# Optimization experiments

Measured on AMD Instinct MI355X. Metric: run time of the kernel, lower is better.

The kernel has to match this reference:

```python
import jax, jax.numpy as jnp
import numpy as np

PATCH_LEN = 16


def _forward(x, W_proj, b_proj, W_router, b_router, W_experts, b_experts, W_head, b_head):
    # x: (B, L, C); Model drops first 2 channels
    seq_len = x.shape[1]
    xs = x[:, :, 2:]                                   # (B, L, N)
    B, L, N = xs.shape
    # CI=True: 'b l n -> (b n) l 1' (track as (BN, L) since trailing dim is 1)
    ci = jnp.transpose(xs, (0, 2, 1)).reshape(B * N, L)
    # RevIN-style instance norm (means detached in torch)
    means = jax.lax.stop_gradient(jnp.mean(ci, axis=1, keepdims=True))
    xc = ci - means
    stdev = jnp.sqrt(jnp.var(xc, axis=1, keepdims=True) + 1e-5)  # unbiased=False
    xc = xc / stdev
    # non-overlapping patching: unfold(1, pl, pl)
    p = L // PATCH_LEN
    patches = xc[:, : p * PATCH_LEN].reshape(B * N, p, PATCH_LEN)
    xp = patches @ W_proj.T + b_proj                   # (BN, p, d)
    gates = jax.nn.softmax(xp @ W_router.T + b_router, axis=-1)  # (BN, p, E)
    # soft-routed mixture of linear experts: sum_e gate_e * (xp @ W_e^T + b_e)
    eo = jnp.einsum('tpd,ehd->tpeh', xp, W_experts) + b_experts  # (BN, p, E, d)
    combined = jnp.einsum('tpeh,tpe->tph', eo, gates)            # (BN, p, d)
    d = combined.shape[-1]
    flat = combined.reshape(B * N, p * d)              # '(b n) p d -> b (p d) n', n=1
    if p * d < seq_len:
        flat = jnp.pad(flat, ((0, 0), (0, seq_len - p * d)))
    else:
        flat = flat[:, :seq_len]
    flat = flat * stdev + means                        # de-normalize (BN, L)
    # '(b n) l 1 -> b l n' then 'b l n -> b n l' == reshape to (B, N, L)
    temporal = flat.reshape(B, N, seq_len)
    out = temporal @ W_head.T + b_head                 # linear_head: (B, N, pred)
    out = jnp.transpose(out, (0, 2, 1))[:, :, :1]      # 'b n d -> b d n', keep var 0
    return out


def setup_inputs() -> dict:
    key = jax.random.key(0)
    ks = jax.random.split(key, 12)
    B, L, C = 32, 1024, 34
    d, E, pl, pred = 256, 8, PATCH_LEN, 96
    return {
        'x': jax.random.normal(ks[0], (B, L, C), dtype=jnp.float32),
        'x_mark_enc': jax.random.normal(ks[1], (B, L, 4), dtype=jnp.float32),
        'x_dec': jax.random.normal(ks[2], (B, pred, C), dtype=jnp.float32),
        'x_mark_dec': jax.random.normal(ks[3], (B, pred, 4), dtype=jnp.float32),
        'W_proj': jax.random.normal(ks[4], (d, pl), dtype=jnp.float32) * 0.1,
        'b_proj': jax.random.normal(ks[5], (d,), dtype=jnp.float32) * 0.02,
        'W_router': jax.random.normal(ks[6], (E, d), dtype=jnp.float32) * 0.05,
        'b_router': jax.random.normal(ks[7], (E,), dtype=jnp.float32) * 0.02,
        'W_experts': jax.random.normal(ks[8], (E, d, d), dtype=jnp.float32) * 0.05,
        'b_experts': jax.random.normal(ks[9], (E, d), dtype=jnp.float32) * 0.02,
        'W_head': jax.random.normal(ks[10], (pred, L), dtype=jnp.float32) * 0.03,
        'b_head': jax.random.normal(ks[11], (pred,), dtype=jnp.float32) * 0.02,
    }


def reference(x, x_mark_enc, x_dec, x_mark_dec, W_proj, b_proj, W_router, b_router,
              W_experts, b_experts, W_head, b_head):
    # x_mark_enc, x_dec, x_mark_dec are accepted but unused by Model.forward
    return _forward(x, W_proj, b_proj, W_router, b_router,
                    W_experts, b_experts, W_head, b_head)
```

## Files before the change

kernel.cpp:

```cpp
#include <hip/hip_runtime.h>
#include <math.h>


#define NB 32
#define LSEQ 1024
#define CCH 34
#define NP 4
#define DMODEL 256
#define NEXP 8
#define PRED 96

#define WT_FLOATS    (NEXP * DMODEL * DMODEL)
#define XP_FLOATS    (NB * NP * DMODEL)
#define GATES_FLOATS (NB * NP * NEXP)
#define STATS_FLOATS (NB * 2)
#define FLAT_FLOATS  (NEXP * NB * LSEQ)

__global__ __launch_bounds__(256) void k_stats(
    const float* __restrict__ x,
    const float* __restrict__ W_proj, const float* __restrict__ b_proj,
    const float* __restrict__ W_router, const float* __restrict__ b_router,
    const float* __restrict__ W_experts, float* __restrict__ Wt,
    float* __restrict__ xp_ws, float* __restrict__ gates_ws,
    float* __restrict__ stats_ws, int do_transpose)
{
    const int bid = blockIdx.x;
    const int tid = threadIdx.x;
    const int b = bid;

    __shared__ float tile[64][33];
    __shared__ float xn[LSEQ];
    __shared__ float xp_s[NP * DMODEL];
    __shared__ float red[8];
    __shared__ float lg[32];
    __shared__ float mean_s, rstd_s;

    float v[4];
    if (b < NB) {
        #pragma unroll
        for (int i = 0; i < 4; ++i)
            v[i] = x[(size_t)(b * LSEQ + tid + 256 * i) * CCH + 2];
    }

    if (do_transpose) {
        const int e  = bid >> 5;
        const int h0 = ((bid >> 3) & 3) << 6;
        const int d0 = (bid & 7) << 5;
        const float* src = W_experts + ((size_t)e << 16);
        float*       dst = Wt        + ((size_t)e << 16);
        const int dx = tid & 31, hy = tid >> 5;
        const int hx = tid & 63, dy = tid >> 6;
        #pragma unroll
        for (int i = 0; i < 8; ++i) {
            const int hh = hy + 8 * i;
            tile[hh][dx] = src[(size_t)(h0 + hh) * DMODEL + d0 + dx];
        }
        __syncthreads();
        #pragma unroll
        for (int i = 0; i < 8; ++i) {
            const int dd = dy + 4 * i;
            dst[(size_t)(d0 + dd) * DMODEL + h0 + hx] = tile[hx][dd];
        }
    }

    if (b >= NB) return;

    float s = 0.f, sq = 0.f;
    #pragma unroll
    for (int i = 0; i < 4; ++i) { s += v[i]; sq += v[i] * v[i]; }
    #pragma unroll
    for (int off = 32; off > 0; off >>= 1) {
        s  += __shfl_down(s,  off);
        sq += __shfl_down(sq, off);
    }
    const int wave = tid >> 6;
    if ((tid & 63) == 0) { red[wave * 2] = s; red[wave * 2 + 1] = sq; }
    __syncthreads();
    if (tid == 0) {
        const float S = red[0] + red[2] + red[4] + red[6];
        const float Q = red[1] + red[3] + red[5] + red[7];
        const float mean = S * (1.0f / LSEQ);
        const float var  = Q * (1.0f / LSEQ) - mean * mean;
        const float stdv = sqrtf(var + 1e-5f);
        mean_s = mean;
        rstd_s = 1.0f / stdv;
        stats_ws[b * 2]     = mean;
        stats_ws[b * 2 + 1] = stdv;
    }
    __syncthreads();
    const float mean = mean_s, rstd = rstd_s;
    #pragma unroll
    for (int i = 0; i < 4; ++i)
        xn[tid + 256 * i] = (v[i] - mean) * rstd;
    __syncthreads();

    {
        const int h = tid;
        float wrow[16];
        #pragma unroll
        for (int j = 0; j < 16; ++j) wrow[j] = W_proj[h * 16 + j];
        const float bp = b_proj[h];
        #pragma unroll
        for (int p = 0; p < NP; ++p) {
            float acc = bp;
            #pragma unroll
            for (int j = 0; j < 16; ++j) acc += xn[p * 16 + j] * wrow[j];
            xp_s[p * DMODEL + h] = acc;
            xp_ws[((size_t)b * NP + p) * DMODEL + h] = acc;
        }
    }
    __syncthreads();

    if (tid < 32) {
        const int p = tid >> 3, e = tid & 7;
        float acc = b_router[e];
        const float* wr = W_router + e * DMODEL;
        const float* xp = xp_s + p * DMODEL;
        #pragma unroll 8
        for (int h = 0; h < DMODEL; ++h) acc += xp[h] * wr[h];
        lg[tid] = acc;
    }
    __syncthreads();

    if (tid < NP) {
        const int p = tid;
        float m = -1e30f;
        #pragma unroll
        for (int e = 0; e < NEXP; ++e) m = fmaxf(m, lg[p * 8 + e]);
        float ex[NEXP];
        float sum = 0.f;
        #pragma unroll
        for (int e = 0; e < NEXP; ++e) { ex[e] = expf(lg[p * 8 + e] - m); sum += ex[e]; }
        const float inv = 1.0f / sum;
        #pragma unroll
        for (int e = 0; e < NEXP; ++e)
            gates_ws[((size_t)b * NP + p) * NEXP + e] = ex[e] * inv;
    }
}

__global__ __launch_bounds__(256) void k_expert(
    const float* __restrict__ Wt, const float* __restrict__ b_experts,
    const float* __restrict__ xp_ws, const float* __restrict__ gates_ws,
    float* __restrict__ flat_part)
{
    const int bid = blockIdx.x;
    const int b  = bid >> 5;
    const int r  = bid & 31;
    const int hq = r >> 3;
    const int e  = r & 7;
    const int tid = threadIdx.x;
    const int p  = tid >> 6;
    const int hl = tid & 63;
    const int h  = (hq << 6) + hl;

    __shared__ float xp_s[NP * DMODEL];
    __shared__ float g_s[NP * NEXP];

    #pragma unroll
    for (int i = 0; i < 4; ++i)
        xp_s[tid + 256 * i] = xp_ws[(size_t)b * (NP * DMODEL) + tid + 256 * i];
    if (tid < NP * NEXP) g_s[tid] = gates_ws[(size_t)b * (NP * NEXP) + tid];
    __syncthreads();

    const float* xp = xp_s + (p << 8);
    const float* wt = Wt + ((size_t)e << 16) + h;
    const float bias = b_experts[(e << 8) + h];
    const float gate = g_s[(p << 3) + e];

    float d0 = 0.f, d1 = 0.f, d2 = 0.f, d3 = 0.f;
    #pragma unroll 4
    for (int d = 0; d < DMODEL; d += 4) {
        d0 += wt[(size_t)(d + 0) << 8] * xp[d + 0];
        d1 += wt[(size_t)(d + 1) << 8] * xp[d + 1];
        d2 += wt[(size_t)(d + 2) << 8] * xp[d + 2];
        d3 += wt[(size_t)(d + 3) << 8] * xp[d + 3];
    }
    const float dot = (d0 + d1) + (d2 + d3);
    flat_part[(((size_t)e * NB + b) << 10) + (p << 8) + h] = gate * (dot + bias);
}

__global__ __launch_bounds__(256) void k_expert_direct(
    const float* __restrict__ W, const float* __restrict__ b_experts,
    const float* __restrict__ xp_ws, const float* __restrict__ gates_ws,
    float* __restrict__ flat_part)
{
    const int bid = blockIdx.x;
    const int b  = bid >> 5;
    const int r  = bid & 31;
    const int hq = r >> 3;
    const int e  = r & 7;
    const int tid = threadIdx.x;
    const int p  = tid >> 6;
    const int hl = tid & 63;
    const int h  = (hq << 6) + hl;

    __shared__ float xp_s[NP * DMODEL];
    __shared__ float g_s[NP * NEXP];

    #pragma unroll
    for (int i = 0; i < 4; ++i)
        xp_s[tid + 256 * i] = xp_ws[(size_t)b * (NP * DMODEL) + tid + 256 * i];
    if (tid < NP * NEXP) g_s[tid] = gates_ws[(size_t)b * (NP * NEXP) + tid];
    __syncthreads();

    const float4* xp4 = (const float4*)(xp_s + (p << 8));
    const float4* wrow = (const float4*)(W + (((size_t)e << 8) + h) * DMODEL);
    const float bias = b_experts[(e << 8) + h];
    const float gate = g_s[(p << 3) + e];

    float d0 = 0.f, d1 = 0.f, d2 = 0.f, d3 = 0.f;
    #pragma unroll 4
    for (int d = 0; d < DMODEL / 4; d += 4) {
        float4 w0 = wrow[d + 0], x0 = xp4[d + 0];
        float4 w1 = wrow[d + 1], x1 = xp4[d + 1];
        float4 w2 = wrow[d + 2], x2 = xp4[d + 2];
        float4 w3 = wrow[d + 3], x3 = xp4[d + 3];
        d0 += w0.x * x0.x + w0.y * x0.y + w0.z * x0.z + w0.w * x0.w;
        d1 += w1.x * x1.x + w1.y * x1.y + w1.z * x1.z + w1.w * x1.w;
        d2 += w2.x * x2.x + w2.y * x2.y + w2.z * x2.z + w2.w * x2.w;
        d3 += w3.x * x3.x + w3.y * x3.y + w3.z * x3.z + w3.w * x3.w;
    }
    const float dot = (d0 + d1) + (d2 + d3);
    flat_part[(((size_t)e * NB + b) << 10) + (p << 8) + h] = gate * (dot + bias);
}

__global__ __launch_bounds__(256) void k_head(
    const float* __restrict__ flat_part, const float* __restrict__ stats_ws,
    const float* __restrict__ W_head, const float* __restrict__ b_head,
    float* __restrict__ out)
{
    const int b = blockIdx.x;
    const int tid = threadIdx.x;
    __shared__ float4 f4s[DMODEL];

    const float mean = stats_ws[b * 2];
    const float stdv = stats_ws[b * 2 + 1];

    {
        float4 acc = make_float4(0.f, 0.f, 0.f, 0.f);
        #pragma unroll
        for (int e = 0; e < NEXP; ++e) {
            const float4 t = ((const float4*)(flat_part + (((size_t)e * NB + b) << 10)))[tid];
            acc.x += t.x; acc.y += t.y; acc.z += t.z; acc.w += t.w;
        }
        acc.x = acc.x * stdv + mean;
        acc.y = acc.y * stdv + mean;
        acc.z = acc.z * stdv + mean;
        acc.w = acc.w * stdv + mean;
        f4s[tid] = acc;
    }
    __syncthreads();

    const int lane = tid & 63;
    const int w    = tid >> 6;

    float4 fr[4];
    #pragma unroll
    for (int c = 0; c < 4; ++c) fr[c] = f4s[lane + 64 * c];

    #pragma unroll 2
    for (int i = 0; i < PRED / 4; ++i) {
        const int k = w + 4 * i;
        const float4* wr = (const float4*)(W_head + (size_t)k * LSEQ);
        float a = 0.f;
        #pragma unroll
        for (int c = 0; c < 4; ++c) {
            const float4 t = wr[lane + 64 * c];
            a += t.x * fr[c].x + t.y * fr[c].y + t.z * fr[c].z + t.w * fr[c].w;
        }
        #pragma unroll
        for (int off = 32; off > 0; off >>= 1)
            a += __shfl_xor(a, off);
        if (lane == 0)
            out[(size_t)b * PRED + k] = b_head[k] + a;
    }
}

extern "C" void kernel_launch(void* const* d_in, const int* in_sizes, int n_in,
                              void* d_out, int out_size, void* d_ws, size_t ws_size,
                              hipStream_t stream)
{
    const float* x         = (const float*)d_in[0];
    const float* W_proj    = (const float*)d_in[4];
    const float* b_proj    = (const float*)d_in[5];
    const float* W_router  = (const float*)d_in[6];
    const float* b_router  = (const float*)d_in[7];
    const float* W_experts = (const float*)d_in[8];
    const float* b_experts = (const float*)d_in[9];
    const float* W_head    = (const float*)d_in[10];
    const float* b_head    = (const float*)d_in[11];
    float* out = (float*)d_out;
    float* ws  = (float*)d_ws;

    const size_t need = (size_t)(WT_FLOATS + XP_FLOATS + GATES_FLOATS +
                                 STATS_FLOATS + FLAT_FLOATS);
    const bool use_t = ws_size >= need * sizeof(float);

    size_t off = use_t ? (size_t)WT_FLOATS : 0;
    float* Wt        = ws;
    float* xp_ws     = ws + off;  off += XP_FLOATS;
    float* gates_ws  = ws + off;  off += GATES_FLOATS;
    float* stats_ws  = ws + off;  off += STATS_FLOATS;
    float* flat_part = ws + off;

    k_stats<<<256, 256, 0, stream>>>(x, W_proj, b_proj, W_router, b_router,
                                     W_experts, Wt, xp_ws, gates_ws, stats_ws,
                                     use_t ? 1 : 0);
    if (use_t) {
        k_expert<<<1024, 256, 0, stream>>>(Wt, b_experts, xp_ws, gates_ws, flat_part);
    } else {
        k_expert_direct<<<1024, 256, 0, stream>>>(W_experts, b_experts,
                                                  xp_ws, gates_ws, flat_part);
    }
    k_head<<<NB, 256, 0, stream>>>(flat_part, stats_ws, W_head, b_head, out);
}
```

Before: 114.5 us.

## Fuse stats, projection, routing and expert matmul into one kernel per (expert,batch)

Merges the stats/projection/router kernel and the expert kernel into one 1024-thread kernel, one block per (expert, batch) pair. Each block recomputes normalization, patch projection and gating for its batch row, then does the expert dot products straight from row-major W_experts. This drops the W_experts transpose pass, the xp/gates workspace round trip and one launch. In exchange the stats/projection/router work is repeated 8 times per batch, and the expert weights are read with per-thread row strides rather than coalesced transposed reads.

```diff
diff --git a/kernel.cpp b/kernel.cpp
--- a/kernel.cpp
+++ b/kernel.cpp
@@ -10,75 +10,46 @@
 #define NEXP 8
 #define PRED 96
 
-#define WT_FLOATS    (NEXP * DMODEL * DMODEL)
-#define XP_FLOATS    (NB * NP * DMODEL)
-#define GATES_FLOATS (NB * NP * NEXP)
 #define STATS_FLOATS (NB * 2)
 #define FLAT_FLOATS  (NEXP * NB * LSEQ)
 
-__global__ __launch_bounds__(256) void k_stats(
+__global__ __launch_bounds__(1024) void k_expert_stats(
     const float* __restrict__ x,
     const float* __restrict__ W_proj, const float* __restrict__ b_proj,
     const float* __restrict__ W_router, const float* __restrict__ b_router,
-    const float* __restrict__ W_experts, float* __restrict__ Wt,
-    float* __restrict__ xp_ws, float* __restrict__ gates_ws,
-    float* __restrict__ stats_ws, int do_transpose)
+    const float* __restrict__ W_experts, const float* __restrict__ b_experts,
+    float* __restrict__ stats_ws, float* __restrict__ flat_part)
 {
     const int bid = blockIdx.x;
+    const int e = bid >> 5;
+    const int b = bid & 31;
     const int tid = threadIdx.x;
-    const int b = bid;
-
-    __shared__ float tile[64][33];
+    const int p = tid >> 8;
+    const int h = tid & 255;
+
     __shared__ float xn[LSEQ];
     __shared__ float xp_s[NP * DMODEL];
-    __shared__ float red[8];
+    __shared__ float red[32];
     __shared__ float lg[32];
+    __shared__ float gate_s[NP];
     __shared__ float mean_s, rstd_s;
 
-    float v[4];
-    if (b < NB) {
-        #pragma unroll
-        for (int i = 0; i < 4; ++i)
-            v[i] = x[(size_t)(b * LSEQ + tid + 256 * i) * CCH + 2];
-    }
-
-    if (do_transpose) {
-        const int e  = bid >> 5;
-        const int h0 = ((bid >> 3) & 3) << 6;
-        const int d0 = (bid & 7) << 5;
-        const float* src = W_experts + ((size_t)e << 16);
-        float*       dst = Wt        + ((size_t)e << 16);
-        const int dx = tid & 31, hy = tid >> 5;
-        const int hx = tid & 63, dy = tid >> 6;
-        #pragma unroll
-        for (int i = 0; i < 8; ++i) {
-            const int hh = hy + 8 * i;
-            tile[hh][dx] = src[(size_t)(h0 + hh) * DMODEL + d0 + dx];
-        }
-        __syncthreads();
-        #pragma unroll
-        for (int i = 0; i < 8; ++i) {
-            const int dd = dy + 4 * i;
-            dst[(size_t)(d0 + dd) * DMODEL + h0 + hx] = tile[hx][dd];
-        }
-    }
-
-    if (b >= NB) return;
-
-    float s = 0.f, sq = 0.f;
-    #pragma unroll
-    for (int i = 0; i < 4; ++i) { s += v[i]; sq += v[i] * v[i]; }
-    #pragma unroll
-    for (int off = 32; off > 0; off >>= 1) {
-        s  += __shfl_down(s,  off);
-        sq += __shfl_down(sq, off);
-    }
-    const int wave = tid >> 6;
-    if ((tid & 63) == 0) { red[wave * 2] = s; red[wave * 2 + 1] = sq; }
+    const float v = x[(size_t)(b * LSEQ + tid) * CCH + 2];
+    {
+        float s = v, sq = v * v;
+        #pragma unroll
+        for (int off = 32; off > 0; off >>= 1) {
+            s  += __shfl_down(s,  off);
+            sq += __shfl_down(sq, off);
+        }
+        const int wave = tid >> 6;
+        if ((tid & 63) == 0) { red[wave * 2] = s; red[wave * 2 + 1] = sq; }
+    }
     __syncthreads();
     if (tid == 0) {
-        const float S = red[0] + red[2] + red[4] + red[6];
-        const float Q = red[1] + red[3] + red[5] + red[7];
+        float S = 0.f, Q = 0.f;
+        #pragma unroll
+        for (int w = 0; w < 16; ++w) { S += red[w * 2]; Q += red[w * 2 + 1]; }
         const float mean = S * (1.0f / LSEQ);
         const float var  = Q * (1.0f / LSEQ) - mean * mean;
         const float stdv = sqrtf(var + 1e-5f);
@@ -88,140 +59,76 @@
         stats_ws[b * 2 + 1] = stdv;
     }
     __syncthreads();
-    const float mean = mean_s, rstd = rstd_s;
-    #pragma unroll
-    for (int i = 0; i < 4; ++i)
-        xn[tid + 256 * i] = (v[i] - mean) * rstd;
-    __syncthreads();
-
-    {
-        const int h = tid;
-        float wrow[16];
-        #pragma unroll
-        for (int j = 0; j < 16; ++j) wrow[j] = W_proj[h * 16 + j];
-        const float bp = b_proj[h];
-        #pragma unroll
-        for (int p = 0; p < NP; ++p) {
-            float acc = bp;
-            #pragma unroll
-            for (int j = 0; j < 16; ++j) acc += xn[p * 16 + j] * wrow[j];
-            xp_s[p * DMODEL + h] = acc;
-            xp_ws[((size_t)b * NP + p) * DMODEL + h] = acc;
-        }
-    }
-    __syncthreads();
-
-    if (tid < 32) {
-        const int p = tid >> 3, e = tid & 7;
-        float acc = b_router[e];
-        const float* wr = W_router + e * DMODEL;
-        const float* xp = xp_s + p * DMODEL;
-        #pragma unroll 8
-        for (int h = 0; h < DMODEL; ++h) acc += xp[h] * wr[h];
-        lg[tid] = acc;
+    xn[tid] = (v - mean_s) * rstd_s;
+    __syncthreads();
+
+    {
+        const float4* wp = (const float4*)(W_proj + h * 16);
+        float acc = b_proj[h];
+        #pragma unroll
+        for (int j4 = 0; j4 < 4; ++j4) {
+            const float4 w = wp[j4];
+            acc += xn[p * 16 + j4 * 4 + 0] * w.x;
+            acc += xn[p * 16 + j4 * 4 + 1] * w.y;
+            acc += xn[p * 16 + j4 * 4 + 2] * w.z;
+            acc += xn[p * 16 + j4 * 4 + 3] * w.w;
+        }
+        xp_s[(p << 8) + h] = acc;
+    }
+    __syncthreads();
+
+    {
+        const int er = (tid >> 5) & 7;
+        const int c  = tid & 31;
+        const float* xp = xp_s + (p << 8);
+        const float* wr = W_router + er * DMODEL;
+        float a = 0.f;
+        #pragma unroll
+        for (int jj = 0; jj < 8; ++jj)
+            a += xp[c + 32 * jj] * wr[c + 32 * jj];
+        #pragma unroll
+        for (int off = 16; off > 0; off >>= 1)
+            a += __shfl_xor(a, off);
+        if (c == 0) lg[(p << 3) + er] = a + b_router[er];
     }
     __syncthreads();
 
     if (tid < NP) {
-        const int p = tid;
+        const int pp = tid;
         float m = -1e30f;
         #pragma unroll
-        for (int e = 0; e < NEXP; ++e) m = fmaxf(m, lg[p * 8 + e]);
-        float ex[NEXP];
+        for (int ee = 0; ee < NEXP; ++ee) m = fmaxf(m, lg[pp * 8 + ee]);
         float sum = 0.f;
-        #pragma unroll
-        for (int e = 0; e < NEXP; ++e) { ex[e] = expf(lg[p * 8 + e] - m); sum += ex[e]; }
-        const float inv = 1.0f / sum;
-        #pragma unroll
-        for (int e = 0; e < NEXP; ++e)
-            gates_ws[((size_t)b * NP + p) * NEXP + e] = ex[e] * inv;
-    }
-}
-
-__global__ __launch_bounds__(256) void k_expert(
-    const float* __restrict__ Wt, const float* __restrict__ b_experts,
-    const float* __restrict__ xp_ws, const float* __restrict__ gates_ws,
-    float* __restrict__ flat_part)
-{
-    const int bid = blockIdx.x;
-    const int b  = bid >> 5;
-    const int r  = bid & 31;
-    const int hq = r >> 3;
-    const int e  = r & 7;
-    const int tid = threadIdx.x;
-    const int p  = tid >> 6;
-    const int hl = tid & 63;
-    const int h  = (hq << 6) + hl;
-
-    __shared__ float xp_s[NP * DMODEL];
-    __shared__ float g_s[NP * NEXP];
-
-    #pragma unroll
-    for (int i = 0; i < 4; ++i)
-        xp_s[tid + 256 * i] = xp_ws[(size_t)b * (NP * DMODEL) + tid + 256 * i];
-    if (tid < NP * NEXP) g_s[tid] = gates_ws[(size_t)b * (NP * NEXP) + tid];
-    __syncthreads();
-
-    const float* xp = xp_s + (p << 8);
-    const float* wt = Wt + ((size_t)e << 16) + h;
-    const float bias = b_experts[(e << 8) + h];
-    const float gate = g_s[(p << 3) + e];
-
-    float d0 = 0.f, d1 = 0.f, d2 = 0.f, d3 = 0.f;
-    #pragma unroll 4
-    for (int d = 0; d < DMODEL; d += 4) {
-        d0 += wt[(size_t)(d + 0) << 8] * xp[d + 0];
-        d1 += wt[(size_t)(d + 1) << 8] * xp[d + 1];
-        d2 += wt[(size_t)(d + 2) << 8] * xp[d + 2];
-        d3 += wt[(size_t)(d + 3) << 8] * xp[d + 3];
-    }
-    const float dot = (d0 + d1) + (d2 + d3);
-    flat_part[(((size_t)e * NB + b) << 10) + (p << 8) + h] = gate * (dot + bias);
-}
-
-__global__ __launch_bounds__(256) void k_expert_direct(
-    const float* __restrict__ W, const float* __restrict__ b_experts,
-    const float* __restrict__ xp_ws, const float* __restrict__ gates_ws,
-    float* __restrict__ flat_part)
-{
-    const int bid = blockIdx.x;
-    const int b  = bid >> 5;
-    const int r  = bid & 31;
-    const int hq = r >> 3;
-    const int e  = r & 7;
-    const int tid = threadIdx.x;
-    const int p  = tid >> 6;
-    const int hl = tid & 63;
-    const int h  = (hq << 6) + hl;
-
-    __shared__ float xp_s[NP * DMODEL];
-    __shared__ float g_s[NP * NEXP];
-
-    #pragma unroll
-    for (int i = 0; i < 4; ++i)
-        xp_s[tid + 256 * i] = xp_ws[(size_t)b * (NP * DMODEL) + tid + 256 * i];
-    if (tid < NP * NEXP) g_s[tid] = gates_ws[(size_t)b * (NP * NEXP) + tid];
-    __syncthreads();
-
-    const float4* xp4 = (const float4*)(xp_s + (p << 8));
-    const float4* wrow = (const float4*)(W + (((size_t)e << 8) + h) * DMODEL);
-    const float bias = b_experts[(e << 8) + h];
-    const float gate = g_s[(p << 3) + e];
-
-    float d0 = 0.f, d1 = 0.f, d2 = 0.f, d3 = 0.f;
-    #pragma unroll 4
-    for (int d = 0; d < DMODEL / 4; d += 4) {
-        float4 w0 = wrow[d + 0], x0 = xp4[d + 0];
-        float4 w1 = wrow[d + 1], x1 = xp4[d + 1];
-        float4 w2 = wrow[d + 2], x2 = xp4[d + 2];
-        float4 w3 = wrow[d + 3], x3 = xp4[d + 3];
-        d0 += w0.x * x0.x + w0.y * x0.y + w0.z * x0.z + w0.w * x0.w;
-        d1 += w1.x * x1.x + w1.y * x1.y + w1.z * x1.z + w1.w * x1.w;
-        d2 += w2.x * x2.x + w2.y * x2.y + w2.z * x2.z + w2.w * x2.w;
-        d3 += w3.x * x3.x + w3.y * x3.y + w3.z * x3.z + w3.w * x3.w;
-    }
-    const float dot = (d0 + d1) + (d2 + d3);
-    flat_part[(((size_t)e * NB + b) << 10) + (p << 8) + h] = gate * (dot + bias);
+        float my = 0.f;
+        #pragma unroll
+        for (int ee = 0; ee < NEXP; ++ee) {
+            const float ex = expf(lg[pp * 8 + ee] - m);
+            sum += ex;
+            if (ee == e) my = ex;
+        }
+        gate_s[pp] = my / sum;
+    }
+    __syncthreads();
+
+    {
+        const float4* wrow = (const float4*)(W_experts + (((size_t)e << 8) + h) * DMODEL);
+        const float4* xp4  = (const float4*)(xp_s + (p << 8));
+        float d0 = 0.f, d1 = 0.f, d2 = 0.f, d3 = 0.f;
+        #pragma unroll 4
+        for (int d = 0; d < DMODEL / 4; d += 4) {
+            float4 w0 = wrow[d + 0], x0 = xp4[d + 0];
+            float4 w1 = wrow[d + 1], x1 = xp4[d + 1];
+            float4 w2 = wrow[d + 2], x2 = xp4[d + 2];
+            float4 w3 = wrow[d + 3], x3 = xp4[d + 3];
+            d0 += w0.x * x0.x + w0.y * x0.y + w0.z * x0.z + w0.w * x0.w;
+            d1 += w1.x * x1.x + w1.y * x1.y + w1.z * x1.z + w1.w * x1.w;
+            d2 += w2.x * x2.x + w2.y * x2.y + w2.z * x2.z + w2.w * x2.w;
+            d3 += w3.x * x3.x + w3.y * x3.y + w3.z * x3.z + w3.w * x3.w;
+        }
+        const float dot = (d0 + d1) + (d2 + d3);
+        flat_part[(((size_t)e * NB + b) << 10) + (p << 8) + h] =
+            gate_s[p] * (dot + b_experts[(e << 8) + h]);
+    }
 }
 
 __global__ __launch_bounds__(256) void k_head(
@@ -253,7 +160,6 @@
 
     const int lane = tid & 63;
     const int w    = tid >> 6;
-
     float4 fr[4];
     #pragma unroll
     for (int c = 0; c < 4; ++c) fr[c] = f4s[lane + 64 * c];
@@ -292,25 +198,11 @@
     float* out = (float*)d_out;
     float* ws  = (float*)d_ws;
 
-    const size_t need = (size_t)(WT_FLOATS + XP_FLOATS + GATES_FLOATS +
-                                 STATS_FLOATS + FLAT_FLOATS);
-    const bool use_t = ws_size >= need * sizeof(float);
-
-    size_t off = use_t ? (size_t)WT_FLOATS : 0;
-    float* Wt        = ws;
-    float* xp_ws     = ws + off;  off += XP_FLOATS;
-    float* gates_ws  = ws + off;  off += GATES_FLOATS;
-    float* stats_ws  = ws + off;  off += STATS_FLOATS;
-    float* flat_part = ws + off;
-
-    k_stats<<<256, 256, 0, stream>>>(x, W_proj, b_proj, W_router, b_router,
-                                     W_experts, Wt, xp_ws, gates_ws, stats_ws,
-                                     use_t ? 1 : 0);
-    if (use_t) {
-        k_expert<<<1024, 256, 0, stream>>>(Wt, b_experts, xp_ws, gates_ws, flat_part);
-    } else {
-        k_expert_direct<<<1024, 256, 0, stream>>>(W_experts, b_experts,
-                                                  xp_ws, gates_ws, flat_part);
-    }
+    float* stats_ws  = ws;
+    float* flat_part = ws + STATS_FLOATS;
+
+    k_expert_stats<<<256, 1024, 0, stream>>>(
+        x, W_proj, b_proj, W_router, b_router,
+        W_experts, b_experts, stats_ws, flat_part);
     k_head<<<NB, 256, 0, stream>>>(flat_part, stats_ws, W_head, b_head, out);
 }
```

Measured after the change: 128.5 us. 12.2% more time.
